# Optimization experiments

Measured on AMD Instinct MI355X. Metric: run time of the kernel, lower is better.

Reference implementation:

```python
import jax, jax.numpy as jnp
import numpy as np

N_NODES = 50000
N_EDGES = 400000
IN_CH = 814
HID = 128
HEADS1 = 4
NUM_CLASSES = 46
NUM_GRAPHS = 64
NEG_SLOPE = 0.2


def setup_inputs() -> dict:
    key = jax.random.key(0)
    ks = jax.random.split(key, 16)
    x = jax.random.normal(ks[0], (N_NODES, IN_CH), dtype=jnp.float32)
    edge_index = jax.random.randint(ks[1], (2, N_EDGES), 0, N_NODES, dtype=jnp.int32)
    batch = jnp.sort(jax.random.randint(ks[2], (N_NODES,), 0, NUM_GRAPHS, dtype=jnp.int32))
    s = 0.05
    # GATConv 1: in 814 -> 4 heads x 128, concat
    W1 = jax.random.normal(ks[3], (IN_CH, HEADS1 * HID), dtype=jnp.float32) * s
    a_src1 = jax.random.normal(ks[4], (HEADS1, HID), dtype=jnp.float32) * s
    a_dst1 = jax.random.normal(ks[5], (HEADS1, HID), dtype=jnp.float32) * s
    b1 = jnp.zeros((HEADS1 * HID,), dtype=jnp.float32)
    # GATConv 2: in 512 -> 1 head x 128, no concat (mean)
    W2 = jax.random.normal(ks[6], (HEADS1 * HID, HID), dtype=jnp.float32) * s
    a_src2 = jax.random.normal(ks[7], (1, HID), dtype=jnp.float32) * s
    a_dst2 = jax.random.normal(ks[8], (1, HID), dtype=jnp.float32) * s
    b2 = jnp.zeros((HID,), dtype=jnp.float32)
    # MLP head 128 -> 64 -> 46 (dropout is identity in eval mode)
    fc1_w = jax.random.normal(ks[9], (HID, 64), dtype=jnp.float32) * s
    fc1_b = jnp.zeros((64,), dtype=jnp.float32)
    fc2_w = jax.random.normal(ks[10], (64, NUM_CLASSES), dtype=jnp.float32) * s
    fc2_b = jnp.zeros((NUM_CLASSES,), dtype=jnp.float32)
    return {"x": x, "edge_index": edge_index, "batch": batch,
            "W1": W1, "a_src1": a_src1, "a_dst1": a_dst1, "b1": b1,
            "W2": W2, "a_src2": a_src2, "a_dst2": a_dst2, "b2": b2,
            "fc1_w": fc1_w, "fc1_b": fc1_b, "fc2_w": fc2_w, "fc2_b": fc2_b}


def _gat_layer(x, src, dst, W, a_src, a_dst, bias, heads, out_ch, concat):
    # PyG GATConv: linear transform, edge attention w/ LeakyReLU,
    # segment softmax over destination nodes, scatter-add aggregation.
    n = x.shape[0]
    h = (x @ W).reshape(n, heads, out_ch)                 # [N,H,C]
    al_s = jnp.einsum('nhc,hc->nh', h, a_src)             # [N,H]
    al_d = jnp.einsum('nhc,hc->nh', h, a_dst)             # [N,H]
    e = jax.nn.leaky_relu(al_s[src] + al_d[dst], NEG_SLOPE)  # [E,H]
    m = jax.ops.segment_max(e, dst, num_segments=n)       # [N,H]
    ex = jnp.exp(e - m[dst])
    denom = jax.ops.segment_sum(ex, dst, num_segments=n)  # [N,H]
    alpha = ex / denom[dst]                               # [E,H]
    out = jax.ops.segment_sum(h[src] * alpha[:, :, None], dst, num_segments=n)  # [N,H,C]
    if concat:
        return out.reshape(n, heads * out_ch) + bias
    return out.mean(axis=1) + bias


def reference(x, edge_index, batch, W1, a_src1, a_dst1, b1,
              W2, a_src2, a_dst2, b2, fc1_w, fc1_b, fc2_w, fc2_b):
    n = x.shape[0]
    # GATConv adds self-loops by default
    loops = jnp.arange(n, dtype=edge_index.dtype)
    src = jnp.concatenate([edge_index[0], loops])
    dst = jnp.concatenate([edge_index[1], loops])
    h = jax.nn.relu(_gat_layer(x, src, dst, W1, a_src1, a_dst1, b1, HEADS1, HID, True))
    h = jax.nn.relu(_gat_layer(h, src, dst, W2, a_src2, a_dst2, b2, 1, HID, False))
    # global mean pool over graphs
    sums = jax.ops.segment_sum(h, batch, num_segments=NUM_GRAPHS)      # [G,128]
    cnts = jax.ops.segment_sum(jnp.ones((n,), h.dtype), batch, num_segments=NUM_GRAPHS)
    pooled = sums / jnp.maximum(cnts, 1.0)[:, None]
    # MLP head (dropout = identity at inference)
    z = jax.nn.relu(pooled @ fc1_w + fc1_b)
    return z @ fc2_w + fc2_b
```

## Files before the change

### kernel.cpp

```cpp
#include <hip/hip_runtime.h>
#include <hip/hip_bf16.h>

#define N_NODES 50000
#define N_EDGES 400000
#define IN_CH   814
#define HID     128
#define HEADS1  4
#define NUM_GRAPHS 64
#define NUM_CLASSES 46
#define NEG_SLOPE 0.2f
#define KP 832

typedef __attribute__((ext_vector_type(8))) short bf16x8;
typedef __attribute__((ext_vector_type(4))) float f32x4;

__device__ __forceinline__ float leaky(float v) { return v > 0.f ? v : NEG_SLOPE * v; }

__device__ __forceinline__ unsigned short f2bf(float f) {
  unsigned u = __float_as_uint(f);
  unsigned r = u + 0x7fff + ((u >> 16) & 1);
  return (unsigned short)(r >> 16);
}
__device__ __forceinline__ float bf2f(short s) {
  return __uint_as_float(((unsigned)(unsigned short)s) << 16);
}

#define GLOAD_LDS16(g, l)                                                        \
  __builtin_amdgcn_global_load_lds((const __attribute__((address_space(1))) unsigned*)(g), \
                                   (__attribute__((address_space(3))) unsigned*)(l), 16, 0, 0)

__global__ __launch_bounds__(256) void convert_x(const float* __restrict__ x,
                                                 unsigned short* __restrict__ Ab) {
  const int row = blockIdx.x;
  const int c = threadIdx.x * 4;
  if (c >= KP) return;
  const float* xr = x + (size_t)row * IN_CH;
  float v[4] = {0.f, 0.f, 0.f, 0.f};
  if (c + 3 < IN_CH) {
    float2 u0 = *(const float2*)(xr + c);
    float2 u1 = *(const float2*)(xr + c + 2);
    v[0] = u0.x; v[1] = u0.y; v[2] = u1.x; v[3] = u1.y;
  } else {
#pragma unroll
    for (int k = 0; k < 4; k++) if (c + k < IN_CH) v[k] = xr[c + k];
  }
  ushort4 o = make_ushort4(f2bf(v[0]), f2bf(v[1]), f2bf(v[2]), f2bf(v[3]));
  *(ushort4*)&Ab[(size_t)row * KP + c] = o;
}

__global__ __launch_bounds__(256) void convert_w1t(const float* __restrict__ W1,
                                                   unsigned short* __restrict__ Bt) {
  __shared__ float tile[32][33];
  const int n0 = blockIdx.x * 32;
  const int k0 = blockIdx.y * 32;
  const int tx = threadIdx.x & 31, ty = threadIdx.x >> 5;
#pragma unroll
  for (int i = 0; i < 32; i += 8) {
    const int k = k0 + ty + i;
    tile[ty + i][tx] = (k < IN_CH) ? W1[(size_t)k * 512 + n0 + tx] : 0.f;
  }
  __syncthreads();
#pragma unroll
  for (int i = 0; i < 32; i += 8) {
    const int n = n0 + ty + i;
    Bt[(size_t)n * KP + k0 + tx] = f2bf(tile[tx][ty + i]);
  }
}

__global__ __launch_bounds__(256) void convert_w2t(const float* __restrict__ W2,
                                                   unsigned short* __restrict__ Bt2) {
  const int n = blockIdx.x;
  unsigned short* br = Bt2 + (size_t)n * 512;
  for (int k = threadIdx.x; k < 512; k += 256) br[k] = f2bf(W2[(size_t)k * 128 + n]);
}

template<int KPITCH, int CPITCH, bool OUTBF>
__global__ __launch_bounds__(256) void gemm_mfma(const unsigned short* __restrict__ A,
                                                 const unsigned short* __restrict__ B,
                                                 void* __restrict__ Cv) {
  constexpr int NT = KPITCH / 64;
  __shared__ unsigned short sA[2][8 * 128 * 8];
  __shared__ unsigned short sB[2][8 * 128 * 8];
  const int tid = threadIdx.x;
  const int w = tid >> 6, lane = tid & 63;
  const int row0 = blockIdx.y * 128;
  const int col0 = blockIdx.x * 128;
  const int wr = w >> 1, wc = w & 1;

  f32x4 acc[4][4];
#pragma unroll
  for (int mi = 0; mi < 4; mi++)
#pragma unroll
    for (int nj = 0; nj < 4; nj++) acc[mi][nj] = (f32x4){0.f, 0.f, 0.f, 0.f};

  long a_off[4], b_off[4];
  int lds_base[4];
#pragma unroll
  for (int c = 0; c < 4; c++) {
    const int s = (w * 4 + c) * 64 + lane;
    const int kg = s >> 7, r = s & 127;
    int arow = row0 + r; if (arow >= N_NODES) arow = N_NODES - 1;
    a_off[c] = (long)arow * KPITCH + kg * 8;
    b_off[c] = (long)(col0 + r) * KPITCH + kg * 8;
    lds_base[c] = (w * 4 + c) * 64 * 8;
  }
  int aoff[4][2], boff[4][2];
#pragma unroll
  for (int i = 0; i < 4; i++)
#pragma unroll
    for (int ks = 0; ks < 2; ks++) {
      aoff[i][ks] = ((ks * 4 + (lane >> 4)) * 128 + wr * 64 + i * 16 + (lane & 15)) * 8;
      boff[i][ks] = ((ks * 4 + (lane >> 4)) * 128 + wc * 64 + i * 16 + (lane & 15)) * 8;
    }

#define STAGE(kt, b)                                                     \
  {                                                                      \
    const int kbase = (kt) * 64;                                         \
    _Pragma("unroll")                                                    \
    for (int c = 0; c < 4; c++) {                                        \
      GLOAD_LDS16(A + (a_off[c] + kbase), &sA[b][lds_base[c]]);          \
      GLOAD_LDS16(B + (b_off[c] + kbase), &sB[b][lds_base[c]]);          \
    }                                                                    \
  }

#define COMPUTE(b)                                                                   \
  {                                                                                  \
    bf16x8 af[4][2], bfr[4][2];                                                      \
    _Pragma("unroll")                                                                \
    for (int mi = 0; mi < 4; mi++)                                                   \
      _Pragma("unroll")                                                              \
      for (int ks = 0; ks < 2; ks++) af[mi][ks] = *(const bf16x8*)&sA[b][aoff[mi][ks]]; \
    _Pragma("unroll")                                                                \
    for (int nj = 0; nj < 4; nj++)                                                   \
      _Pragma("unroll")                                                              \
      for (int ks = 0; ks < 2; ks++) bfr[nj][ks] = *(const bf16x8*)&sB[b][boff[nj][ks]]; \
    _Pragma("unroll")                                                                \
    for (int mi = 0; mi < 4; mi++)                                                   \
      _Pragma("unroll")                                                              \
      for (int nj = 0; nj < 4; nj++) {                                               \
        acc[mi][nj] = __builtin_amdgcn_mfma_f32_16x16x32_bf16(af[mi][0], bfr[nj][0], acc[mi][nj], 0, 0, 0); \
        acc[mi][nj] = __builtin_amdgcn_mfma_f32_16x16x32_bf16(af[mi][1], bfr[nj][1], acc[mi][nj], 0, 0, 0); \
      }                                                                              \
  }

  STAGE(0, 0);
  __syncthreads();
  int cur = 0;
  for (int kt = 0; kt < NT - 1; ++kt) {
    STAGE(kt + 1, cur ^ 1);
    COMPUTE(cur);
    __syncthreads();
    cur ^= 1;
  }
  COMPUTE(cur);
#undef STAGE
#undef COMPUTE

  const int r4 = (lane >> 4) * 4;
  const int cc = lane & 15;
#pragma unroll
  for (int mi = 0; mi < 4; mi++) {
#pragma unroll
    for (int r = 0; r < 4; r++) {
      const int gr = row0 + wr * 64 + mi * 16 + r4 + r;
      if (gr < N_NODES) {
        if (OUTBF) {
          unsigned short* cp = (unsigned short*)Cv + (size_t)gr * CPITCH + col0 + wc * 64 + cc;
#pragma unroll
          for (int nj = 0; nj < 4; nj++) cp[nj * 16] = f2bf(acc[mi][nj][r]);
        } else {
          float* cp = (float*)Cv + (size_t)gr * CPITCH + col0 + wc * 64 + cc;
#pragma unroll
          for (int nj = 0; nj < 4; nj++) cp[nj * 16] = acc[mi][nj][r];
        }
      }
    }
  }
}

__global__ __launch_bounds__(256) void attn_prep1(const unsigned short* __restrict__ h1b,
                                                  const float* __restrict__ a_src,
                                                  const float* __restrict__ a_dst,
                                                  float* __restrict__ als,
                                                  float* __restrict__ ald) {
  const int n = blockIdx.x * 4 + (threadIdx.x >> 6);
  const int lane = threadIdx.x & 63;
  if (n >= N_NODES) return;
  const int c0 = lane * 8;
  const bf16x8 hv = *(const bf16x8*)&h1b[(size_t)n * 512 + c0];
  float ps = 0.f, pd = 0.f;
#pragma unroll
  for (int j = 0; j < 8; j++) {
    const float f = bf2f(hv[j]);
    ps += f * a_src[c0 + j];
    pd += f * a_dst[c0 + j];
  }
#pragma unroll
  for (int off = 8; off; off >>= 1) {
    ps += __shfl_xor(ps, off);
    pd += __shfl_xor(pd, off);
  }
  if ((lane & 15) == 0) {
    als[n * 4 + (lane >> 4)] = ps;
    ald[n * 4 + (lane >> 4)] = pd;
  }
}

__global__ __launch_bounds__(256) void attn_prep2(const float* __restrict__ h2,
                                                  const float* __restrict__ a_src,
                                                  const float* __restrict__ a_dst,
                                                  float* __restrict__ als,
                                                  float* __restrict__ ald) {
  const int n = blockIdx.x * 4 + (threadIdx.x >> 6);
  const int lane = threadIdx.x & 63;
  if (n >= N_NODES) return;
  const float* hr = h2 + (size_t)n * 128;
  float h0 = hr[lane], h1v = hr[lane + 64];
  float ps = h0 * a_src[lane] + h1v * a_src[lane + 64];
  float pd = h0 * a_dst[lane] + h1v * a_dst[lane + 64];
#pragma unroll
  for (int off = 32; off; off >>= 1) {
    ps += __shfl_xor(ps, off);
    pd += __shfl_xor(pd, off);
  }
  if (lane == 0) { als[n] = ps; ald[n] = pd; }
}

__global__ void init_misc(int* deg, float* pooled, float* cnts) {
  const int i = blockIdx.x * 256 + threadIdx.x;
  if (i < N_NODES) deg[i] = 1;
  if (i < NUM_GRAPHS * HID) pooled[i] = 0.f;
  if (i < NUM_GRAPHS) cnts[i] = 0.f;
}

__global__ void hist_kernel(const int* __restrict__ dst, int* deg) {
  const int e = blockIdx.x * 256 + threadIdx.x;
  if (e < N_EDGES) atomicAdd(&deg[dst[e]], 1);
}

__global__ __launch_bounds__(256) void scan_block_sum(const int* __restrict__ deg, int* bsum) {
  __shared__ int sd[256];
  const int t = threadIdx.x;
  const int i = blockIdx.x * 256 + t;
  sd[t] = (i < N_NODES) ? deg[i] : 0;
  __syncthreads();
  for (int s = 128; s; s >>= 1) { if (t < s) sd[t] += sd[t + s]; __syncthreads(); }
  if (t == 0) bsum[blockIdx.x] = sd[0];
}

__global__ __launch_bounds__(256) void scan_base(const int* __restrict__ bsum, int* bbase, int* offsets) {
  __shared__ int tmp[256];
  const int t = threadIdx.x;
  const int nb = (N_NODES + 255) / 256;
  const int v = (t < nb) ? bsum[t] : 0;
  tmp[t] = v;
  __syncthreads();
  for (int off = 1; off < 256; off <<= 1) {
    int a = (t >= off) ? tmp[t - off] : 0;
    __syncthreads();
    tmp[t] += a;
    __syncthreads();
  }
  if (t < nb) bbase[t] = tmp[t] - v;
  if (t == 255) offsets[N_NODES] = tmp[255];
}

__global__ __launch_bounds__(256) void scan_final(const int* __restrict__ deg,
                                                  const int* __restrict__ bbase,
                                                  int* offsets, int* cursor) {
  __shared__ int tmp[256];
  const int t = threadIdx.x;
  const int i = blockIdx.x * 256 + t;
  const int v = (i < N_NODES) ? deg[i] : 0;
  tmp[t] = v;
  __syncthreads();
  for (int off = 1; off < 256; off <<= 1) {
    int a = (t >= off) ? tmp[t - off] : 0;
    __syncthreads();
    tmp[t] += a;
    __syncthreads();
  }
  if (i < N_NODES) {
    const int excl = bbase[blockIdx.x] + tmp[t] - v;
    offsets[i] = excl;
    cursor[i] = excl;
  }
}

__global__ void scatter_kernel(const int* __restrict__ src, const int* __restrict__ dst,
                               int* cursor, int* __restrict__ srcs) {
  const int e = blockIdx.x * 256 + threadIdx.x;
  if (e >= N_EDGES + N_NODES) return;
  int s, d;
  if (e < N_EDGES) { s = src[e]; d = dst[e]; }
  else { s = e - N_EDGES; d = s; }
  const int p = atomicAdd(&cursor[d], 1);
  srcs[p] = s;
}

__global__ __launch_bounds__(256) void aggregate1(const unsigned short* __restrict__ h1b,
                                                  const float* __restrict__ als,
                                                  const float* __restrict__ ald,
                                                  const int* __restrict__ offsets,
                                                  const int* __restrict__ srcs,
                                                  const float* __restrict__ b1,
                                                  unsigned short* __restrict__ x2b) {
  const int n = blockIdx.x * 4 + (threadIdx.x >> 6);
  const int lane = threadIdx.x & 63;
  if (n >= N_NODES) return;
  const int beg = offsets[n], end = offsets[n + 1];
  const int h = lane >> 4;
  const int c0 = lane * 8;
  const float aldh = ald[n * 4 + h];
  float m = -1e30f;
  for (int p = beg; p < end; p++)
    m = fmaxf(m, leaky(als[srcs[p] * 4 + h] + aldh));
  float den = 0.f;
  float acc[8] = {0, 0, 0, 0, 0, 0, 0, 0};
  for (int p = beg; p < end; p++) {
    const int s = srcs[p];
    const float w = __expf(leaky(als[s * 4 + h] + aldh) - m);
    den += w;
    const bf16x8 hv = *(const bf16x8*)&h1b[(size_t)s * 512 + c0];
#pragma unroll
    for (int j = 0; j < 8; j++) acc[j] += w * bf2f(hv[j]);
  }
  bf16x8 o;
  const float inv = 1.f / den;
#pragma unroll
  for (int j = 0; j < 8; j++)
    o[j] = (short)f2bf(fmaxf(acc[j] * inv + b1[c0 + j], 0.f));
  *(bf16x8*)&x2b[(size_t)n * 512 + c0] = o;
}

__global__ __launch_bounds__(256) void aggregate2(const float* __restrict__ h2,
                                                  const float* __restrict__ als,
                                                  const float* __restrict__ ald,
                                                  const int* __restrict__ offsets,
                                                  const int* __restrict__ srcs,
                                                  const float* __restrict__ b2,
                                                  float* __restrict__ out2) {
  const int n = blockIdx.x * 4 + (threadIdx.x >> 6);
  const int lane = threadIdx.x & 63;
  if (n >= N_NODES) return;
  const int beg = offsets[n], end = offsets[n + 1];
  const int c0 = lane * 2;
  const float aldn = ald[n];
  float m = -1e30f;
  for (int p = beg; p < end; p++) m = fmaxf(m, leaky(als[srcs[p]] + aldn));
  float den = 0.f, a0 = 0.f, a1 = 0.f;
  for (int p = beg; p < end; p++) {
    const int s = srcs[p];
    const float w = __expf(leaky(als[s] + aldn) - m);
    den += w;
    const float2 hv = *(const float2*)&h2[(size_t)s * 128 + c0];
    a0 += w * hv.x;
    a1 += w * hv.y;
  }
  const float inv = 1.f / den;
  float2 o = make_float2(fmaxf(a0 * inv + b2[c0], 0.f), fmaxf(a1 * inv + b2[c0 + 1], 0.f));
  *(float2*)&out2[(size_t)n * 128 + c0] = o;
}

__global__ __launch_bounds__(128) void pool_kernel(const float* __restrict__ out2,
                                                   const int* __restrict__ batch,
                                                   float* pooled, float* cnts) {
  const int t = threadIdx.x;
  const int base = blockIdx.x * 256;
  float acc = 0.f;
  float cnt = 0.f;
  int cur = -1;
  for (int i = 0; i < 256; i++) {
    const int n = base + i;
    if (n >= N_NODES) break;
    const int g = batch[n];
    if (g != cur) {
      if (cur >= 0) {
        atomicAdd(&pooled[cur * HID + t], acc);
        if (t == 0) atomicAdd(&cnts[cur], cnt);
      }
      acc = 0.f; cnt = 0.f; cur = g;
    }
    acc += out2[(size_t)n * HID + t];
    cnt += 1.f;
  }
  if (cur >= 0) {
    atomicAdd(&pooled[cur * HID + t], acc);
    if (t == 0) atomicAdd(&cnts[cur], cnt);
  }
}

__global__ __launch_bounds__(64) void mlp_kernel(const float* __restrict__ pooled,
                                                 const float* __restrict__ cnts,
                                                 const float* __restrict__ fc1_w,
                                                 const float* __restrict__ fc1_b,
                                                 const float* __restrict__ fc2_w,
                                                 const float* __restrict__ fc2_b,
                                                 float* __restrict__ out) {
  __shared__ float pl[128];
  __shared__ float z[64];
  const int g = blockIdx.x, t = threadIdx.x;
  const float c = fmaxf(cnts[g], 1.0f);
  pl[t] = pooled[g * HID + t] / c;
  pl[t + 64] = pooled[g * HID + t + 64] / c;
  __syncthreads();
  float acc = fc1_b[t];
  for (int i = 0; i < 128; i++) acc += pl[i] * fc1_w[i * 64 + t];
  z[t] = fmaxf(acc, 0.f);
  __syncthreads();
  if (t < NUM_CLASSES) {
    float o = fc2_b[t];
    for (int i = 0; i < 64; i++) o += z[i] * fc2_w[i * NUM_CLASSES + t];
    out[g * NUM_CLASSES + t] = o;
  }
}

extern "C" void kernel_launch(void* const* d_in, const int* in_sizes, int n_in,
                              void* d_out, int out_size, void* d_ws, size_t ws_size,
                              hipStream_t stream) {
  const float* x       = (const float*)d_in[0];
  const int*   ei      = (const int*)d_in[1];
  const int*   batch   = (const int*)d_in[2];
  const float* W1      = (const float*)d_in[3];
  const float* a_src1  = (const float*)d_in[4];
  const float* a_dst1  = (const float*)d_in[5];
  const float* b1      = (const float*)d_in[6];
  const float* W2      = (const float*)d_in[7];
  const float* a_src2  = (const float*)d_in[8];
  const float* a_dst2  = (const float*)d_in[9];
  const float* b2      = (const float*)d_in[10];
  const float* fc1_w   = (const float*)d_in[11];
  const float* fc1_b   = (const float*)d_in[12];
  const float* fc2_w   = (const float*)d_in[13];
  const float* fc2_b   = (const float*)d_in[14];
  float* out = (float*)d_out;

  const int* e_src = ei;
  const int* e_dst = ei + N_EDGES;

  float* wsf = (float*)d_ws;
  unsigned short* h1b = (unsigned short*)wsf;
  unsigned short* Ab  = (unsigned short*)(wsf + 12800000);
  unsigned short* x2b = (unsigned short*)(wsf + 33600000);
  unsigned short* Bt  = (unsigned short*)(wsf + 46400000);
  unsigned short* Bt2 = (unsigned short*)(wsf + 46613000);
  float* als1 = wsf + 46646000;
  float* ald1 = als1 + 200000;
  float* als2 = ald1 + 200000;
  float* ald2 = als2 + 50000;
  float* pooled = ald2 + 50000;
  float* cnts = pooled + 8192;
  int* deg     = (int*)(cnts + 64);
  int* offsets = deg + 50000;
  int* cursor  = offsets + 50001;
  int* srcs    = cursor + 50000;
  int* bsum    = srcs + 450000;
  int* bbase   = bsum + 200;
  float* h2   = wsf + 12800000;
  float* out2 = wsf + 19200000;

  const int NB = (N_NODES + 255) / 256;

  init_misc<<<NB, 256, 0, stream>>>(deg, pooled, cnts);
  hist_kernel<<<(N_EDGES + 255) / 256, 256, 0, stream>>>(e_dst, deg);
  scan_block_sum<<<NB, 256, 0, stream>>>(deg, bsum);
  scan_base<<<1, 256, 0, stream>>>(bsum, bbase, offsets);
  scan_final<<<NB, 256, 0, stream>>>(deg, bbase, offsets, cursor);
  scatter_kernel<<<(N_EDGES + N_NODES + 255) / 256, 256, 0, stream>>>(e_src, e_dst, cursor, srcs);

  convert_x<<<N_NODES, 256, 0, stream>>>(x, Ab);
  convert_w1t<<<dim3(16, 26), 256, 0, stream>>>(W1, Bt);
  gemm_mfma<KP, 512, true><<<dim3(4, 391), 256, 0, stream>>>(Ab, Bt, (void*)h1b);
  attn_prep1<<<12500, 256, 0, stream>>>(h1b, a_src1, a_dst1, als1, ald1);
  aggregate1<<<12500, 256, 0, stream>>>(h1b, als1, ald1, offsets, srcs, b1, x2b);

  convert_w2t<<<128, 256, 0, stream>>>(W2, Bt2);
  gemm_mfma<512, 128, false><<<dim3(1, 391), 256, 0, stream>>>(x2b, Bt2, (void*)h2);
  attn_prep2<<<12500, 256, 0, stream>>>(h2, a_src2, a_dst2, als2, ald2);
  aggregate2<<<12500, 256, 0, stream>>>(h2, als2, ald2, offsets, srcs, b2, out2);

  pool_kernel<<<NB, 128, 0, stream>>>(out2, batch, pooled, cnts);
  mlp_kernel<<<NUM_GRAPHS, 64, 0, stream>>>(pooled, cnts, fc1_w, fc1_b, fc2_w, fc2_b, out);
}
```

Before: 742.2 us.

## Fuse attention-logit projections into GEMM epilogue and deepen K-loop prefetch

Removes the separate attn_prep1/attn_prep2 kernels by computing the per-node source and destination attention dot products from the GEMM accumulators in the epilogue. Partial sums are reduced across lanes and through LDS into als/ald. It also restructures the K loop to prefetch two stages ahead, using explicit vmcnt waits and raw barriers instead of __syncthreads. This saves re-reading h1/h2 and two launches. The cost is hand-placed waitcnt logic that must match the load count per STAGE. Logits now come from fp32 accumulators rather than the bf16-rounded h1, so the numerics shift slightly.

```diff
diff --git a/kernel.cpp b/kernel.cpp
--- a/kernel.cpp
+++ b/kernel.cpp
@@ -77,7 +77,11 @@
 template<int KPITCH, int CPITCH, bool OUTBF>
 __global__ __launch_bounds__(256) void gemm_mfma(const unsigned short* __restrict__ A,
                                                  const unsigned short* __restrict__ B,
-                                                 void* __restrict__ Cv) {
+                                                 void* __restrict__ Cv,
+                                                 const float* __restrict__ as_,
+                                                 const float* __restrict__ ad_,
+                                                 float* __restrict__ als,
+                                                 float* __restrict__ ald) {
   constexpr int NT = KPITCH / 64;
   __shared__ unsigned short sA[2][8 * 128 * 8];
   __shared__ unsigned short sB[2][8 * 128 * 8];
@@ -144,15 +148,25 @@
   }
 
   STAGE(0, 0);
-  __syncthreads();
+  STAGE(1, 1);
   int cur = 0;
-  for (int kt = 0; kt < NT - 1; ++kt) {
-    STAGE(kt + 1, cur ^ 1);
+  for (int kt = 0; kt < NT; ++kt) {
+    if (kt < NT - 1) {
+      asm volatile("s_waitcnt vmcnt(8)" ::: "memory");
+    } else {
+      asm volatile("s_waitcnt vmcnt(0)" ::: "memory");
+    }
+    __builtin_amdgcn_s_barrier();
+    __builtin_amdgcn_sched_barrier(0);
     COMPUTE(cur);
-    __syncthreads();
+    if (kt + 2 < NT) {
+      asm volatile("s_waitcnt lgkmcnt(0)" ::: "memory");
+      __builtin_amdgcn_s_barrier();
+      __builtin_amdgcn_sched_barrier(0);
+      STAGE(kt + 2, cur);
+    }
     cur ^= 1;
   }
-  COMPUTE(cur);
 #undef STAGE
 #undef COMPUTE
 
@@ -176,54 +190,43 @@
       }
     }
   }
-}
-
-__global__ __launch_bounds__(256) void attn_prep1(const unsigned short* __restrict__ h1b,
-                                                  const float* __restrict__ a_src,
-                                                  const float* __restrict__ a_dst,
-                                                  float* __restrict__ als,
-                                                  float* __restrict__ ald) {
-  const int n = blockIdx.x * 4 + (threadIdx.x >> 6);
-  const int lane = threadIdx.x & 63;
-  if (n >= N_NODES) return;
-  const int c0 = lane * 8;
-  const bf16x8 hv = *(const bf16x8*)&h1b[(size_t)n * 512 + c0];
-  float ps = 0.f, pd = 0.f;
-#pragma unroll
-  for (int j = 0; j < 8; j++) {
-    const float f = bf2f(hv[j]);
-    ps += f * a_src[c0 + j];
-    pd += f * a_dst[c0 + j];
-  }
-#pragma unroll
-  for (int off = 8; off; off >>= 1) {
-    ps += __shfl_xor(ps, off);
-    pd += __shfl_xor(pd, off);
-  }
-  if ((lane & 15) == 0) {
-    als[n * 4 + (lane >> 4)] = ps;
-    ald[n * 4 + (lane >> 4)] = pd;
-  }
-}
-
-__global__ __launch_bounds__(256) void attn_prep2(const float* __restrict__ h2,
-                                                  const float* __restrict__ a_src,
-                                                  const float* __restrict__ a_dst,
-                                                  float* __restrict__ als,
-                                                  float* __restrict__ ald) {
-  const int n = blockIdx.x * 4 + (threadIdx.x >> 6);
-  const int lane = threadIdx.x & 63;
-  if (n >= N_NODES) return;
-  const float* hr = h2 + (size_t)n * 128;
-  float h0 = hr[lane], h1v = hr[lane + 64];
-  float ps = h0 * a_src[lane] + h1v * a_src[lane + 64];
-  float pd = h0 * a_dst[lane] + h1v * a_dst[lane + 64];
-#pragma unroll
-  for (int off = 32; off; off >>= 1) {
-    ps += __shfl_xor(ps, off);
-    pd += __shfl_xor(pd, off);
-  }
-  if (lane == 0) { als[n] = ps; ald[n] = pd; }
+
+  __syncthreads();
+  float* pld = (float*)sA;
+#pragma unroll
+  for (int mi = 0; mi < 4; mi++) {
+#pragma unroll
+    for (int r = 0; r < 4; r++) {
+      float s = 0.f, d = 0.f;
+#pragma unroll
+      for (int nj = 0; nj < 4; nj++) {
+        const float v = acc[mi][nj][r];
+        const int gc = col0 + wc * 64 + nj * 16 + cc;
+        s += v * as_[gc];
+        d += v * ad_[gc];
+      }
+#pragma unroll
+      for (int off = 8; off; off >>= 1) {
+        s += __shfl_xor(s, off);
+        d += __shfl_xor(d, off);
+      }
+      if ((lane & 15) == 0) {
+        const int rowL = wr * 64 + mi * 16 + r4 + r;
+        pld[0 * 256 + wc * 128 + rowL] = s;
+        pld[1 * 256 + wc * 128 + rowL] = d;
+      }
+    }
+  }
+  __syncthreads();
+  if (tid < 128) {
+    const int gr = row0 + tid;
+    if (gr < N_NODES) {
+      constexpr int NH = CPITCH / 128;
+      const int hd = col0 >> 7;
+      als[(size_t)gr * NH + hd] = pld[tid] + pld[128 + tid];
+      ald[(size_t)gr * NH + hd] = pld[256 + tid] + pld[256 + 128 + tid];
+    }
+  }
 }
 
 __global__ void init_misc(int* deg, float* pooled, float* cnts) {
@@ -470,13 +473,13 @@
 
   convert_x<<<N_NODES, 256, 0, stream>>>(x, Ab);
   convert_w1t<<<dim3(16, 26), 256, 0, stream>>>(W1, Bt);
-  gemm_mfma<KP, 512, true><<<dim3(4, 391), 256, 0, stream>>>(Ab, Bt, (void*)h1b);
-  attn_prep1<<<12500, 256, 0, stream>>>(h1b, a_src1, a_dst1, als1, ald1);
+  gemm_mfma<KP, 512, true><<<dim3(4, 391), 256, 0, stream>>>(Ab, Bt, (void*)h1b,
+                                                             a_src1, a_dst1, als1, ald1);
   aggregate1<<<12500, 256, 0, stream>>>(h1b, als1, ald1, offsets, srcs, b1, x2b);
 
   convert_w2t<<<128, 256, 0, stream>>>(W2, Bt2);
-  gemm_mfma<512, 128, false><<<dim3(1, 391), 256, 0, stream>>>(x2b, Bt2, (void*)h2);
-  attn_prep2<<<12500, 256, 0, stream>>>(h2, a_src2, a_dst2, als2, ald2);
+  gemm_mfma<512, 128, false><<<dim3(1, 391), 256, 0, stream>>>(x2b, Bt2, (void*)h2,
+                                                               a_src2, a_dst2, als2, ald2);
   aggregate2<<<12500, 256, 0, stream>>>(h2, als2, ald2, offsets, srcs, b2, out2);
 
   pool_kernel<<<NB, 128, 0, stream>>>(out2, batch, pooled, cnts);
```

After: 726.4 us. -2.1%, faster.
